# Performance work log

Hardware: AMD Instinct MI355X
Metric: run time of the kernel (lower is better)

The kernel has to match this reference:

```python
import jax, jax.numpy as jnp
import numpy as np

N_SRC = 8192
N_DST = 8192
E = 524288
D = 128
M = 64


def layer_norm(x, g, b, eps=1e-5):
    mu = x.mean(-1, keepdims=True)
    var = ((x - mu) ** 2).mean(-1, keepdims=True)
    return (x - mu) * jax.lax.rsqrt(var + eps) * g + b


def setup_inputs() -> dict:
    key = jax.random.key(0)
    ks = jax.random.split(key, 32)

    def p(k, shape, s=0.02):
        return jax.random.normal(k, shape, jnp.float32) * s

    inp = {
        "src_embed": jax.random.normal(ks[0], (N_SRC, D), jnp.float32),
        "dst_embed": jax.random.normal(ks[1], (N_DST, D), jnp.float32),
        "v_s2d": jax.random.normal(ks[2], (E, M), jnp.float32),
        "v_d2s": jax.random.normal(ks[3], (E, M), jnp.float32),
        "e_s2d_dst": jax.random.randint(ks[4], (E,), 0, N_DST, jnp.int32),
        "e_d2s_dst": jax.random.randint(ks[5], (E,), 0, N_SRC, jnp.int32),
        # node transforms
        "W_src": p(ks[6], (D, D)), "b_src": jnp.zeros((D,), jnp.float32),
        "W_dst": p(ks[7], (D, D)), "b_dst": jnp.zeros((D,), jnp.float32),
        # edge-message transforms
        "W_sm": p(ks[8], (M, D)), "b_sm": jnp.zeros((D,), jnp.float32),
        "W_dm": p(ks[9], (M, D)), "b_dm": jnp.zeros((D,), jnp.float32),
        # apply_row: LNLayer (Linear+LayerNorm) then Linear
        "row_W1": p(ks[10], (D, D)), "row_b1": jnp.zeros((D,), jnp.float32),
        "row_g": jnp.ones((D,), jnp.float32), "row_beta": jnp.zeros((D,), jnp.float32),
        "row_W2": p(ks[11], (D, D)), "row_b2": jnp.zeros((D,), jnp.float32),
        # apply_col
        "col_W1": p(ks[12], (D, D)), "col_b1": jnp.zeros((D,), jnp.float32),
        "col_g": jnp.ones((D,), jnp.float32), "col_beta": jnp.zeros((D,), jnp.float32),
        "col_W2": p(ks[13], (D, D)), "col_b2": jnp.zeros((D,), jnp.float32),
    }
    return inp


def reference(src_embed, dst_embed, v_s2d, v_d2s, e_s2d_dst, e_d2s_dst,
              W_src, b_src, W_dst, b_dst, W_sm, b_sm, W_dm, b_dm,
              row_W1, row_b1, row_g, row_beta, row_W2, row_b2,
              col_W1, col_b1, col_g, col_beta, col_W2, col_b2):
    # node transforms: h[ntype]
    h_src = src_embed @ W_src + b_src          # [N_src, D]
    h_dst = dst_embed @ W_dst + b_dst          # [N_dst, D]
    # edge message transforms
    msg_s2d = v_s2d @ W_sm + b_sm              # [E, D]
    msg_d2s = v_d2s @ W_dm + b_dm              # [E, D]
    # message = h[dst-of-edge] * msg, scatter-sum onto destination nodes
    out_dst = jax.ops.segment_sum(h_dst[e_s2d_dst] * msg_s2d, e_s2d_dst,
                                  num_segments=N_DST)   # src2dst -> dst nodes
    out_src = jax.ops.segment_sum(h_src[e_d2s_dst] * msg_d2s, e_d2s_dst,
                                  num_segments=N_SRC)   # dst2src -> src nodes
    # residual apply: x + Linear(LayerNorm(Linear(out)))
    row = src_embed + (layer_norm(out_src @ row_W1 + row_b1, row_g, row_beta) @ row_W2 + row_b2)
    col = dst_embed + (layer_norm(out_dst @ col_W1 + col_b1, col_g, col_beta) @ col_W2 + col_b2)
    return row, col
```

## Files before the change

### kernel.cpp

```cpp
#include <hip/hip_runtime.h>


#define DEV __device__ __forceinline__

typedef __bf16 bf16x8 __attribute__((ext_vector_type(8)));
typedef unsigned short u16x8 __attribute__((ext_vector_type(8)));
typedef unsigned short u16x4 __attribute__((ext_vector_type(4)));
typedef float f32x4 __attribute__((ext_vector_type(4)));

constexpr int N_NODES = 8192;
constexpr int NUM_E   = 524288;
constexpr int D       = 128;
constexpr int M       = 64;
constexpr int CAP     = 128;

DEV unsigned short f2bf(float f) {
    unsigned int x = __float_as_uint(f);
    unsigned int r = (x + 0x7fffu + ((x >> 16) & 1u)) >> 16;
    return (unsigned short)r;
}
DEV bf16x8 load8(const unsigned short* p) {
    return *reinterpret_cast<const bf16x8*>(p);
}
DEV bf16x8 cvt8(const float* p) {
    union { u16x8 u; bf16x8 b; } cv;
#pragma unroll
    for (int i = 0; i < 8; ++i) cv.u[i] = f2bf(p[i]);
    return cv.b;
}
DEV f32x4 b2f4(u16x4 u) {
    f32x4 r;
#pragma unroll
    for (int i = 0; i < 4; ++i) r[i] = __uint_as_float((unsigned)u[i] << 16);
    return r;
}
DEV f32x4 mfma16(bf16x8 a, bf16x8 b, f32x4 c) {
    return __builtin_amdgcn_mfma_f32_16x16x32_bf16(a, b, c, 0, 0, 0);
}

struct TransArgs {
    const float* src[8];
    unsigned short* dst[8];
    int K[8];
};
__global__ __launch_bounds__(256) void transpose_k(TransArgs ta, int* __restrict__ cursors) {
    int b = blockIdx.x;
    if (b >= 8) {
        int z = b - 8;
        int4 zero = {0, 0, 0, 0};
        int4* p = reinterpret_cast<int4*>(cursors) + (size_t)z * 1024 + threadIdx.x;
#pragma unroll
        for (int q = 0; q < 4; ++q) p[q * 256] = zero;
        return;
    }
    const float* s = ta.src[b];
    unsigned short* d = ta.dst[b];
    int K = ta.K[b];
    int total = K << 7;
    for (int i = threadIdx.x; i < total; i += 256) {
        int k = i >> 7, n = i & 127;
        d[n * K + k] = f2bf(s[i]);
    }
}

__global__ __launch_bounds__(256) void convscat_k(const float* __restrict__ v0,
                                                  const float* __restrict__ v1,
                                                  const int* __restrict__ i0,
                                                  const int* __restrict__ i1,
                                                  int* __restrict__ cursors,
                                                  int* __restrict__ bucket,
                                                  unsigned short* __restrict__ vb) {
    int b = blockIdx.x;
    if (b < 1024) {
        int t = b * 256 + threadIdx.x;
        int dir = 0;
        if (t >= NUM_E / 4) { dir = 1; t -= NUM_E / 4; }
        const int4* idx = (const int4*)(dir ? i1 : i0);
        int4 nn = idx[t];
        int* cur = cursors + dir * N_NODES;
        int* bk = bucket + (size_t)dir * N_NODES * CAP;
        int e = t * 4;
        int a = nn.x & (N_NODES - 1), c = nn.y & (N_NODES - 1);
        int f = nn.z & (N_NODES - 1), h = nn.w & (N_NODES - 1);
        int pa = atomicAdd(cur + a, 1); if (pa < CAP) bk[a * CAP + pa] = e;
        int pc = atomicAdd(cur + c, 1); if (pc < CAP) bk[c * CAP + pc] = e + 1;
        int pf = atomicAdd(cur + f, 1); if (pf < CAP) bk[f * CAP + pf] = e + 2;
        int ph = atomicAdd(cur + h, 1); if (ph < CAP) bk[h * CAP + ph] = e + 3;
        return;
    }
    int cb = b - 1024;
    const float* vsrc = (cb < 1024) ? v0 : v1;
    unsigned short* vdst = vb + (cb < 1024 ? 0 : (size_t)NUM_E * M);
    size_t base = (size_t)(cb & 1023) * 32768;
#pragma unroll
    for (int q = 0; q < 32; ++q) {
        size_t i = base + ((size_t)q * 256 + threadIdx.x) * 4;
        f32x4 x = *(const f32x4*)(vsrc + i);
        union { unsigned short u[4]; unsigned long long ll; } y;
#pragma unroll
        for (int k = 0; k < 4; ++k) y.u[k] = f2bf(x[k]);
        *reinterpret_cast<unsigned long long*>(vdst + i) = y.ll;
    }
}

struct SideArgs {
    const float* X;
    const unsigned short* vb;
    const int* bucket;
    const int* counts;
    const unsigned short* Wnode_t;
    const float* bnode;
    const unsigned short* Wmsg_t;
    const float* bmsg;
    const unsigned short* W1_t;
    const float* b1;
    const float* g;
    const float* beta;
    const unsigned short* W2_t;
    const float* b2;
    float* out;
};

__global__ __launch_bounds__(256) void apply_k(SideArgs A0, SideArgs A1) {
    const int side = blockIdx.x >> 9;
    const SideArgs& a = side ? A1 : A0;
    const int grp = blockIdx.x & 511;
    const int nb = grp * 16;
    const int w = threadIdx.x >> 6;
    const int lane = threadIdx.x & 63;
    const int m = lane & 15;
    const int quad = lane >> 4;

    __shared__ __align__(16) unsigned short sA[16 * 72];
    __shared__ __align__(16) unsigned short sP[16 * 136];
    __shared__ float part_s[4][16], part_sq[4][16];

    {
        const int f16 = lane & 15;
        const int g = lane >> 4;
        for (int nd = 0; nd < 4; ++nd) {
            int n = nb + 4 * w + nd;
            const int* list = a.bucket + (size_t)n * CAP;
            int deg = a.counts[n];
            int degc = deg < CAP ? deg : CAP;
            f32x4 acc = {0.f, 0.f, 0.f, 0.f};
            int nfull = degc >> 4;
            int j = 0;
            if (nfull > 0) {
                int i0 = list[g], i1 = list[g + 4];
                int i2 = list[g + 8], i3 = list[g + 12];
                for (int it = 0; it < nfull; ++it) {
                    int jn = j + 16;
                    int p0 = 0, p1 = 0, p2 = 0, p3 = 0;
                    if ((it + 1) < nfull) {
                        p0 = list[jn + g];
                        p1 = list[jn + g + 4];
                        p2 = list[jn + g + 8];
                        p3 = list[jn + g + 12];
                    }
                    u16x4 d0 = *(const u16x4*)(a.vb + (size_t)i0 * M + f16 * 4);
                    u16x4 d1 = *(const u16x4*)(a.vb + (size_t)i1 * M + f16 * 4);
                    u16x4 d2 = *(const u16x4*)(a.vb + (size_t)i2 * M + f16 * 4);
                    u16x4 d3 = *(const u16x4*)(a.vb + (size_t)i3 * M + f16 * 4);
                    acc += b2f4(d0); acc += b2f4(d1);
                    acc += b2f4(d2); acc += b2f4(d3);
                    i0 = p0; i1 = p1; i2 = p2; i3 = p3;
                    j = jn;
                }
            }
            for (; j < degc; j += 4) {
                int e = j + g;
                if (e < degc)
                    acc += b2f4(*(const u16x4*)(a.vb + (size_t)list[e] * M + f16 * 4));
            }
#pragma unroll
            for (int i = 0; i < 4; ++i) {
                acc[i] += __shfl_xor(acc[i], 16, 64);
                acc[i] += __shfl_xor(acc[i], 32, 64);
            }
            if (g == 0) {
                union { unsigned short u[4]; unsigned long long ll; } wv;
#pragma unroll
                for (int i = 0; i < 4; ++i) wv.u[i] = f2bf(acc[i]);
                *reinterpret_cast<unsigned long long*>(sA + (4 * w + nd) * 72 + f16 * 4) = wv.ll;
            }
        }
    }

    bf16x8 af[4];
#pragma unroll
    for (int ks = 0; ks < 4; ++ks)
        af[ks] = cvt8(a.X + (size_t)(nb + m) * D + ks * 32 + quad * 8);
    f32x4 acc_h[2] = {{0.f, 0.f, 0.f, 0.f}, {0.f, 0.f, 0.f, 0.f}};
#pragma unroll
    for (int i = 0; i < 2; ++i) {
        int dt = 2 * w + i;
#pragma unroll
        for (int ks = 0; ks < 4; ++ks) {
            bf16x8 bfr = load8(a.Wnode_t + (size_t)(dt * 16 + m) * D + ks * 32 + quad * 8);
            acc_h[i] = mfma16(af[ks], bfr, acc_h[i]);
        }
    }
    __syncthreads();

    bf16x8 at[2];
#pragma unroll
    for (int ks = 0; ks < 2; ++ks)
        at[ks] = load8(sA + m * 72 + ks * 32 + quad * 8);
    f32x4 acc_t[2] = {{0.f, 0.f, 0.f, 0.f}, {0.f, 0.f, 0.f, 0.f}};
#pragma unroll
    for (int i = 0; i < 2; ++i) {
        int dt = 2 * w + i;
#pragma unroll
        for (int ks = 0; ks < 2; ++ks) {
            bf16x8 bfr = load8(a.Wmsg_t + (size_t)(dt * 16 + m) * M + ks * 32 + quad * 8);
            acc_t[i] = mfma16(at[ks], bfr, acc_t[i]);
        }
    }
    {
        float cnt_f[4];
#pragma unroll
        for (int r = 0; r < 4; ++r) cnt_f[r] = (float)a.counts[nb + quad * 4 + r];
#pragma unroll
        for (int i = 0; i < 2; ++i) {
            int dt = 2 * w + i;
            float bn = a.bnode[dt * 16 + m];
            float bm = a.bmsg[dt * 16 + m];
#pragma unroll
            for (int r = 0; r < 4; ++r) {
                float hv = acc_h[i][r] + bn;
                float tv = acc_t[i][r] + cnt_f[r] * bm;
                sP[(quad * 4 + r) * 136 + dt * 16 + m] = f2bf(hv * tv);
            }
        }
    }
    __syncthreads();
    bf16x8 au[4];
#pragma unroll
    for (int ks = 0; ks < 4; ++ks)
        au[ks] = load8(sP + m * 136 + ks * 32 + quad * 8);
    f32x4 acc_u[2] = {{0.f, 0.f, 0.f, 0.f}, {0.f, 0.f, 0.f, 0.f}};
#pragma unroll
    for (int i = 0; i < 2; ++i) {
        int dt = 2 * w + i;
#pragma unroll
        for (int ks = 0; ks < 4; ++ks) {
            bf16x8 bfr = load8(a.W1_t + (size_t)(dt * 16 + m) * D + ks * 32 + quad * 8);
            acc_u[i] = mfma16(au[ks], bfr, acc_u[i]);
        }
    }
    float g_f[2], beta_f[2];
#pragma unroll
    for (int i = 0; i < 2; ++i) {
        int dt = 2 * w + i;
        float b1v = a.b1[dt * 16 + m];
        g_f[i] = a.g[dt * 16 + m];
        beta_f[i] = a.beta[dt * 16 + m];
#pragma unroll
        for (int r = 0; r < 4; ++r) acc_u[i][r] += b1v;
    }
    float s[4], sq[4];
#pragma unroll
    for (int r = 0; r < 4; ++r) { s[r] = 0.f; sq[r] = 0.f; }
#pragma unroll
    for (int i = 0; i < 2; ++i)
#pragma unroll
        for (int r = 0; r < 4; ++r) { float u = acc_u[i][r]; s[r] += u; sq[r] += u * u; }
#pragma unroll
    for (int off = 1; off < 16; off <<= 1) {
#pragma unroll
        for (int r = 0; r < 4; ++r) {
            s[r] += __shfl_xor(s[r], off, 64);
            sq[r] += __shfl_xor(sq[r], off, 64);
        }
    }
    if (m == 0) {
#pragma unroll
        for (int r = 0; r < 4; ++r) {
            part_s[w][quad * 4 + r] = s[r];
            part_sq[w][quad * 4 + r] = sq[r];
        }
    }
    __syncthreads();
    float mu[4], rstd[4];
#pragma unroll
    for (int r = 0; r < 4; ++r) {
        int node = quad * 4 + r;
        float S = part_s[0][node] + part_s[1][node] + part_s[2][node] + part_s[3][node];
        float SQ = part_sq[0][node] + part_sq[1][node] + part_sq[2][node] + part_sq[3][node];
        mu[r] = S * (1.0f / 128.0f);
        float var = SQ * (1.0f / 128.0f) - mu[r] * mu[r];
        rstd[r] = rsqrtf(fmaxf(var, 0.f) + 1e-5f);
    }
#pragma unroll
    for (int i = 0; i < 2; ++i) {
        int dt = 2 * w + i;
#pragma unroll
        for (int r = 0; r < 4; ++r) {
            float ln = (acc_u[i][r] - mu[r]) * rstd[r] * g_f[i] + beta_f[i];
            sP[(quad * 4 + r) * 136 + dt * 16 + m] = f2bf(ln);
        }
    }
    __syncthreads();
    bf16x8 ay[4];
#pragma unroll
    for (int ks = 0; ks < 4; ++ks)
        ay[ks] = load8(sP + m * 136 + ks * 32 + quad * 8);
    f32x4 acc_y[2] = {{0.f, 0.f, 0.f, 0.f}, {0.f, 0.f, 0.f, 0.f}};
#pragma unroll
    for (int i = 0; i < 2; ++i) {
        int dt = 2 * w + i;
#pragma unroll
        for (int ks = 0; ks < 4; ++ks) {
            bf16x8 bfr = load8(a.W2_t + (size_t)(dt * 16 + m) * D + ks * 32 + quad * 8);
            acc_y[i] = mfma16(ay[ks], bfr, acc_y[i]);
        }
    }
#pragma unroll
    for (int i = 0; i < 2; ++i) {
        int dt = 2 * w + i;
        float b2v = a.b2[dt * 16 + m];
#pragma unroll
        for (int r = 0; r < 4; ++r) {
            int node = nb + quad * 4 + r;
            int d = dt * 16 + m;
            float xv = a.X[(size_t)node * D + d];
            a.out[(size_t)node * D + d] = acc_y[i][r] + b2v + xv;
        }
    }
}

extern "C" void kernel_launch(void* const* d_in, const int* in_sizes, int n_in,
                              void* d_out, int out_size, void* d_ws, size_t ws_size,
                              hipStream_t stream) {
    const float* src_embed = (const float*)d_in[0];
    const float* dst_embed = (const float*)d_in[1];
    const float* v_s2d = (const float*)d_in[2];
    const float* v_d2s = (const float*)d_in[3];
    const int* e_s2d = (const int*)d_in[4];
    const int* e_d2s = (const int*)d_in[5];
    const float* W_src = (const float*)d_in[6];
    const float* b_src = (const float*)d_in[7];
    const float* W_dst = (const float*)d_in[8];
    const float* b_dst = (const float*)d_in[9];
    const float* W_sm = (const float*)d_in[10];
    const float* b_sm = (const float*)d_in[11];
    const float* W_dm = (const float*)d_in[12];
    const float* b_dm = (const float*)d_in[13];
    const float* row_W1 = (const float*)d_in[14];
    const float* row_b1 = (const float*)d_in[15];
    const float* row_g = (const float*)d_in[16];
    const float* row_beta = (const float*)d_in[17];
    const float* row_W2 = (const float*)d_in[18];
    const float* row_b2 = (const float*)d_in[19];
    const float* col_W1 = (const float*)d_in[20];
    const float* col_b1 = (const float*)d_in[21];
    const float* col_g = (const float*)d_in[22];
    const float* col_beta = (const float*)d_in[23];
    const float* col_W2 = (const float*)d_in[24];
    const float* col_b2 = (const float*)d_in[25];
    float* out = (float*)d_out;

    char* ws = (char*)d_ws;
    int* cursors = (int*)(ws + 0);
    unsigned short* Wt = (unsigned short*)(ws + 65536);
    int* bucket = (int*)(ws + 294912);
    unsigned short* vb = (unsigned short*)(ws + 8683520);

    TransArgs ta;
    const float* srcs[8] = {W_src, W_dst, W_sm, W_dm, row_W1, row_W2, col_W1, col_W2};
    int Ks[8] = {128, 128, 64, 64, 128, 128, 128, 128};
    int offs[8] = {0, 16384, 32768, 40960, 49152, 65536, 81920, 98304};
    for (int i = 0; i < 8; ++i) { ta.src[i] = srcs[i]; ta.dst[i] = Wt + offs[i]; ta.K[i] = Ks[i]; }
    transpose_k<<<12, 256, 0, stream>>>(ta, cursors);

    convscat_k<<<3072, 256, 0, stream>>>(v_s2d, v_d2s, e_s2d, e_d2s, cursors, bucket, vb);

    SideArgs rowA = {src_embed, vb + (size_t)NUM_E * M, bucket + (size_t)N_NODES * CAP,
                     cursors + N_NODES,
                     Wt + 0, b_src, Wt + 40960, b_dm,
                     Wt + 49152, row_b1, row_g, row_beta, Wt + 65536, row_b2,
                     out};
    SideArgs colA = {dst_embed, vb, bucket, cursors,
                     Wt + 16384, b_dst, Wt + 32768, b_sm,
                     Wt + 81920, col_b1, col_g, col_beta, Wt + 98304, col_b2,
                     out + (size_t)N_NODES * D};
    apply_k<<<1024, 256, 0, stream>>>(rowA, colA);
}
```

Measured before the change: 462.2 us.

## Scatter converted edge rows directly into per-node buckets instead of index lists

Replaces the separate bf16 conversion and index-bucketing pass with one kernel. Each wavefront converts edge feature rows and writes them straight into a per-node contiguous slot claimed by atomic. The aggregation stage then streams contiguous 16-byte rows instead of gathering through an index list, which removes the dependent index loads and the random gathers. In exchange the bf16 writes become scattered, the workspace grows to N*CAP*M per direction, and slot order becomes nondeterministic.

```diff
diff --git a/kernel.cpp b/kernel.cpp
--- a/kernel.cpp
+++ b/kernel.cpp
@@ -5,7 +5,6 @@
 
 typedef __bf16 bf16x8 __attribute__((ext_vector_type(8)));
 typedef unsigned short u16x8 __attribute__((ext_vector_type(8)));
-typedef unsigned short u16x4 __attribute__((ext_vector_type(4)));
 typedef float f32x4 __attribute__((ext_vector_type(4)));
 
 constexpr int N_NODES = 8192;
@@ -27,12 +26,6 @@
 #pragma unroll
     for (int i = 0; i < 8; ++i) cv.u[i] = f2bf(p[i]);
     return cv.b;
-}
-DEV f32x4 b2f4(u16x4 u) {
-    f32x4 r;
-#pragma unroll
-    for (int i = 0; i < 4; ++i) r[i] = __uint_as_float((unsigned)u[i] << 16);
-    return r;
 }
 DEV f32x4 mfma16(bf16x8 a, bf16x8 b, f32x4 c) {
     return __builtin_amdgcn_mfma_f32_16x16x32_bf16(a, b, c, 0, 0, 0);
@@ -63,50 +56,42 @@
     }
 }
 
-__global__ __launch_bounds__(256) void convscat_k(const float* __restrict__ v0,
-                                                  const float* __restrict__ v1,
-                                                  const int* __restrict__ i0,
-                                                  const int* __restrict__ i1,
-                                                  int* __restrict__ cursors,
-                                                  int* __restrict__ bucket,
-                                                  unsigned short* __restrict__ vb) {
-    int b = blockIdx.x;
-    if (b < 1024) {
-        int t = b * 256 + threadIdx.x;
-        int dir = 0;
-        if (t >= NUM_E / 4) { dir = 1; t -= NUM_E / 4; }
-        const int4* idx = (const int4*)(dir ? i1 : i0);
-        int4 nn = idx[t];
-        int* cur = cursors + dir * N_NODES;
-        int* bk = bucket + (size_t)dir * N_NODES * CAP;
-        int e = t * 4;
-        int a = nn.x & (N_NODES - 1), c = nn.y & (N_NODES - 1);
-        int f = nn.z & (N_NODES - 1), h = nn.w & (N_NODES - 1);
-        int pa = atomicAdd(cur + a, 1); if (pa < CAP) bk[a * CAP + pa] = e;
-        int pc = atomicAdd(cur + c, 1); if (pc < CAP) bk[c * CAP + pc] = e + 1;
-        int pf = atomicAdd(cur + f, 1); if (pf < CAP) bk[f * CAP + pf] = e + 2;
-        int ph = atomicAdd(cur + h, 1); if (ph < CAP) bk[h * CAP + ph] = e + 3;
-        return;
-    }
-    int cb = b - 1024;
-    const float* vsrc = (cb < 1024) ? v0 : v1;
-    unsigned short* vdst = vb + (cb < 1024 ? 0 : (size_t)NUM_E * M);
-    size_t base = (size_t)(cb & 1023) * 32768;
-#pragma unroll
-    for (int q = 0; q < 32; ++q) {
-        size_t i = base + ((size_t)q * 256 + threadIdx.x) * 4;
-        f32x4 x = *(const f32x4*)(vsrc + i);
+__global__ __launch_bounds__(256) void rowscat_k(const float* __restrict__ v0,
+                                                 const float* __restrict__ v1,
+                                                 const int* __restrict__ i0,
+                                                 const int* __restrict__ i1,
+                                                 int* __restrict__ cursors,
+                                                 unsigned short* __restrict__ rows) {
+    int wid = (blockIdx.x * 256 + threadIdx.x) >> 6;
+    int lane = threadIdx.x & 63;
+    const int f = lane & 15;
+    const int g = lane >> 4;
+    int dir = wid >> 12;
+    const float* v = dir ? v1 : v0;
+    const int* idx = dir ? i1 : i0;
+    int* cur = cursors + dir * N_NODES;
+    unsigned short* bk = rows + (size_t)dir * N_NODES * CAP * M;
+    int base = (wid & 4095) * 128;
+
+    for (int it = 0; it < 32; ++it) {
+        int e = base + it * 4 + g;
+        int n = idx[e] & (N_NODES - 1);
+        f32x4 x = *(const f32x4*)(v + (size_t)e * M + f * 4);
+        int slot = 0;
+        if (f == 0) slot = atomicAdd(cur + n, 1);
+        slot = __shfl(slot, lane & 48, 64);
         union { unsigned short u[4]; unsigned long long ll; } y;
 #pragma unroll
         for (int k = 0; k < 4; ++k) y.u[k] = f2bf(x[k]);
-        *reinterpret_cast<unsigned long long*>(vdst + i) = y.ll;
+        if (slot < CAP)
+            *reinterpret_cast<unsigned long long*>(
+                bk + ((size_t)n * CAP + slot) * M + f * 4) = y.ll;
     }
 }
 
 struct SideArgs {
     const float* X;
-    const unsigned short* vb;
-    const int* bucket;
+    const unsigned short* rows;
     const int* counts;
     const unsigned short* Wnode_t;
     const float* bnode;
@@ -136,53 +121,32 @@
     __shared__ float part_s[4][16], part_sq[4][16];
 
     {
-        const int f16 = lane & 15;
-        const int g = lane >> 4;
+        const int s8 = lane & 7;
+        const int g8 = lane >> 3;
         for (int nd = 0; nd < 4; ++nd) {
             int n = nb + 4 * w + nd;
-            const int* list = a.bucket + (size_t)n * CAP;
+            const unsigned short* rp = a.rows + (size_t)n * CAP * M;
             int deg = a.counts[n];
             int degc = deg < CAP ? deg : CAP;
-            f32x4 acc = {0.f, 0.f, 0.f, 0.f};
-            int nfull = degc >> 4;
-            int j = 0;
-            if (nfull > 0) {
-                int i0 = list[g], i1 = list[g + 4];
-                int i2 = list[g + 8], i3 = list[g + 12];
-                for (int it = 0; it < nfull; ++it) {
-                    int jn = j + 16;
-                    int p0 = 0, p1 = 0, p2 = 0, p3 = 0;
-                    if ((it + 1) < nfull) {
-                        p0 = list[jn + g];
-                        p1 = list[jn + g + 4];
-                        p2 = list[jn + g + 8];
-                        p3 = list[jn + g + 12];
-                    }
-                    u16x4 d0 = *(const u16x4*)(a.vb + (size_t)i0 * M + f16 * 4);
-                    u16x4 d1 = *(const u16x4*)(a.vb + (size_t)i1 * M + f16 * 4);
-                    u16x4 d2 = *(const u16x4*)(a.vb + (size_t)i2 * M + f16 * 4);
-                    u16x4 d3 = *(const u16x4*)(a.vb + (size_t)i3 * M + f16 * 4);
-                    acc += b2f4(d0); acc += b2f4(d1);
-                    acc += b2f4(d2); acc += b2f4(d3);
-                    i0 = p0; i1 = p1; i2 = p2; i3 = p3;
-                    j = jn;
-                }
+            float ac[8];
+#pragma unroll
+            for (int i = 0; i < 8; ++i) ac[i] = 0.f;
+            for (int j = g8; j < degc; j += 8) {
+                union { bf16x8 b; u16x8 u; } rv;
+                rv.b = load8(rp + (size_t)j * M + s8 * 8);
+#pragma unroll
+                for (int i = 0; i < 8; ++i)
+                    ac[i] += __uint_as_float((unsigned)rv.u[i] << 16);
             }
-            for (; j < degc; j += 4) {
-                int e = j + g;
-                if (e < degc)
-                    acc += b2f4(*(const u16x4*)(a.vb + (size_t)list[e] * M + f16 * 4));
-            }
-#pragma unroll
-            for (int i = 0; i < 4; ++i) {
-                acc[i] += __shfl_xor(acc[i], 16, 64);
-                acc[i] += __shfl_xor(acc[i], 32, 64);
-            }
-            if (g == 0) {
-                union { unsigned short u[4]; unsigned long long ll; } wv;
-#pragma unroll
-                for (int i = 0; i < 4; ++i) wv.u[i] = f2bf(acc[i]);
-                *reinterpret_cast<unsigned long long*>(sA + (4 * w + nd) * 72 + f16 * 4) = wv.ll;
+#pragma unroll
+            for (int off = 8; off < 64; off <<= 1)
+#pragma unroll
+                for (int i = 0; i < 8; ++i) ac[i] += __shfl_xor(ac[i], off, 64);
+            if (lane < 8) {
+                union { unsigned short u[8]; bf16x8 b; } wv;
+#pragma unroll
+                for (int i = 0; i < 8; ++i) wv.u[i] = f2bf(ac[i]);
+                *reinterpret_cast<bf16x8*>(sA + (4 * w + nd) * 72 + s8 * 8) = wv.b;
             }
         }
     }
@@ -364,8 +328,7 @@
     char* ws = (char*)d_ws;
     int* cursors = (int*)(ws + 0);
     unsigned short* Wt = (unsigned short*)(ws + 65536);
-    int* bucket = (int*)(ws + 294912);
-    unsigned short* vb = (unsigned short*)(ws + 8683520);
+    unsigned short* rows = (unsigned short*)(ws + 294912);
 
     TransArgs ta;
     const float* srcs[8] = {W_src, W_dst, W_sm, W_dm, row_W1, row_W2, col_W1, col_W2};
@@ -374,14 +337,13 @@
     for (int i = 0; i < 8; ++i) { ta.src[i] = srcs[i]; ta.dst[i] = Wt + offs[i]; ta.K[i] = Ks[i]; }
     transpose_k<<<12, 256, 0, stream>>>(ta, cursors);
 
-    convscat_k<<<3072, 256, 0, stream>>>(v_s2d, v_d2s, e_s2d, e_d2s, cursors, bucket, vb);
-
-    SideArgs rowA = {src_embed, vb + (size_t)NUM_E * M, bucket + (size_t)N_NODES * CAP,
-                     cursors + N_NODES,
+    rowscat_k<<<2048, 256, 0, stream>>>(v_s2d, v_d2s, e_s2d, e_d2s, cursors, rows);
+
+    SideArgs rowA = {src_embed, rows + (size_t)N_NODES * CAP * M, cursors + N_NODES,
                      Wt + 0, b_src, Wt + 40960, b_dm,
                      Wt + 49152, row_b1, row_g, row_beta, Wt + 65536, row_b2,
                      out};
-    SideArgs colA = {dst_embed, vb, bucket, cursors,
+    SideArgs colA = {dst_embed, rows, cursors,
                      Wt + 16384, b_dst, Wt + 32768, b_sm,
                      Wt + 81920, col_b1, col_g, col_beta, Wt + 98304, col_b2,
                      out + (size_t)N_NODES * D};
```

Measured after the change: 426.1 us. 7.8% less time.
